# Performance work log

Hardware: AMD Instinct MI355X
Metric: run time of the kernel (lower is better)

Reference implementation:

```python
import jax, jax.numpy as jnp
import numpy as np

QUBITS = 8
EMBED_DIM = 512
FFN_DIM = 2048


def setup_inputs() -> dict:
    key = jax.random.key(0)
    k_x, k_p, k_w, k_b = jax.random.split(key, 4)
    x = jax.random.normal(k_x, (16, 4096, EMBED_DIM), dtype=jnp.float32)
    params = jax.random.normal(k_p, (QUBITS, 3), dtype=jnp.float32)
    # nn.Linear(qubits, ffn_dim): weight [ffn_dim, qubits], bias [ffn_dim]
    lim = 1.0 / np.sqrt(QUBITS)
    W = jax.random.uniform(k_w, (FFN_DIM, QUBITS), minval=-lim, maxval=lim, dtype=jnp.float32)
    b = jax.random.uniform(k_b, (FFN_DIM,), minval=-lim, maxval=lim, dtype=jnp.float32)
    return {"x": x, "params": params, "W": W, "b": b}


def reference(x, params, W, b):
    # Each qubit i: |0> -> RX(x[..., i % E]) -> RY(params[i,0]) -> RZ(params[i,1]),
    # RZ leaves <Z> unchanged.
    idx = jnp.arange(QUBITS) % x.shape[-1]          # [Q]
    z = jnp.cos(x[..., idx]) * jnp.cos(params[:, 0])  # [B,S,Q]
    return jnp.einsum('bsq,fq->bsf', z, W) + b        # [B,S,ffn_dim]
```

## Files before the change

kernel.cpp:

```cpp
#include <hip/hip_runtime.h>
#include <math.h>

#define QUBITS 8
#define EMBED 512
#define FFN 2048
#define ROWS_PER_BLOCK 32
#define THREADS 256

using f32x4 = __attribute__((ext_vector_type(4))) float;

__global__ __launch_bounds__(THREADS) void qff_kernel(
    const float* __restrict__ x, const float* __restrict__ params,
    const float* __restrict__ W, const float* __restrict__ b,
    float* __restrict__ out)
{
    __shared__ float z_lds[ROWS_PER_BLOCK][QUBITS];

    const int t = threadIdx.x;
    const long long row0 = (long long)blockIdx.x * ROWS_PER_BLOCK;

    {
        const int r = t >> 3, q = t & 7;
        const float xv = x[(row0 + r) * EMBED + q];
        const float cp = cosf(params[q * 3]);
        z_lds[r][q] = cosf(xv) * cp;
    }
    __syncthreads();

    float w[2][4][QUBITS];
    float bias[2][4];
    #pragma unroll
    for (int k = 0; k < 2; ++k) {
        const int fbase = k * 1024 + t * 4;
        #pragma unroll
        for (int j = 0; j < 4; ++j) {
            const f32x4* wp = (const f32x4*)(W + (size_t)(fbase + j) * QUBITS);
            const f32x4 w0 = wp[0], w1 = wp[1];
            w[k][j][0] = w0.x; w[k][j][1] = w0.y; w[k][j][2] = w0.z; w[k][j][3] = w0.w;
            w[k][j][4] = w1.x; w[k][j][5] = w1.y; w[k][j][6] = w1.z; w[k][j][7] = w1.w;
            bias[k][j] = b[fbase + j];
        }
    }

    float* p = out + row0 * FFN + (size_t)t * 4;

    #pragma unroll 2
    for (int r = 0; r < ROWS_PER_BLOCK; ++r) {
        float z[QUBITS];
        #pragma unroll
        for (int q = 0; q < QUBITS; ++q) z[q] = z_lds[r][q];

        #pragma unroll
        for (int k = 0; k < 2; ++k) {
            float a[4];
            #pragma unroll
            for (int j = 0; j < 4; ++j) {
                float s = bias[k][j];
                #pragma unroll
                for (int q = 0; q < QUBITS; ++q) s = fmaf(z[q], w[k][j][q], s);
                a[j] = s;
            }
            f32x4 acc;
            acc.x = a[0]; acc.y = a[1]; acc.z = a[2]; acc.w = a[3];
            *(f32x4*)(p + k * 1024) = acc;
        }
        p += FFN;
    }
}

extern "C" void kernel_launch(void* const* d_in, const int* in_sizes, int n_in,
                              void* d_out, int out_size, void* d_ws, size_t ws_size,
                              hipStream_t stream) {
    const float* x      = (const float*)d_in[0];
    const float* params = (const float*)d_in[1];
    const float* W      = (const float*)d_in[2];
    const float* b      = (const float*)d_in[3];
    float* out = (float*)d_out;

    const long long rows = (long long)in_sizes[0] / EMBED;
    const int grid = (int)(rows / ROWS_PER_BLOCK);

    qff_kernel<<<grid, THREADS, 0, stream>>>(x, params, W, b, out);
}
```

Baseline: 107.9 us.

## Split cosine prep into separate kernel and use nontemporal output stores

Adds a prep kernel that computes the 8 qubit Z expectations per row into workspace with vectorized loads. A store-focused kernel then reads these compact z values instead of doing strided x gathers and cosines. Both paths switch output writes to nontemporal stores to cut cache pollution on the 512MB output stream, and the unroll pragma is dropped. The cost is an extra launch and a small intermediate buffer round-trip; the fused path remains as a fallback when workspace is too small.

```diff
diff --git a/kernel.cpp b/kernel.cpp
--- a/kernel.cpp
+++ b/kernel.cpp
@@ -9,7 +9,81 @@
 
 using f32x4 = __attribute__((ext_vector_type(4))) float;
 
-__global__ __launch_bounds__(THREADS) void qff_kernel(
+__global__ __launch_bounds__(THREADS) void zprep_kernel(
+    const float* __restrict__ x, const float* __restrict__ params,
+    float* __restrict__ z, long long rows)
+{
+    const long long tid = (long long)blockIdx.x * THREADS + threadIdx.x;
+    const long long row = tid >> 1;
+    if (row >= rows) return;
+    const int half = (int)(tid & 1);
+
+    float cp[4];
+    #pragma unroll
+    for (int j = 0; j < 4; ++j) cp[j] = cosf(params[(half * 4 + j) * 3]);
+
+    const f32x4 xv = *(const f32x4*)(x + row * EMBED + half * 4);
+    f32x4 zv;
+    zv.x = cosf(xv.x) * cp[0];
+    zv.y = cosf(xv.y) * cp[1];
+    zv.z = cosf(xv.z) * cp[2];
+    zv.w = cosf(xv.w) * cp[3];
+    *(f32x4*)(z + row * QUBITS + half * 4) = zv;
+}
+
+__global__ __launch_bounds__(THREADS) void qff_store_kernel(
+    const float* __restrict__ z, const float* __restrict__ W,
+    const float* __restrict__ b, float* __restrict__ out)
+{
+    __shared__ float z_lds[ROWS_PER_BLOCK * QUBITS];
+
+    const int t = threadIdx.x;
+    const long long row0 = (long long)blockIdx.x * ROWS_PER_BLOCK;
+
+    z_lds[t] = z[row0 * QUBITS + t];
+    __syncthreads();
+
+    float w[2][4][QUBITS];
+    float bias[2][4];
+    #pragma unroll
+    for (int k = 0; k < 2; ++k) {
+        const int fbase = k * 1024 + t * 4;
+        #pragma unroll
+        for (int j = 0; j < 4; ++j) {
+            const f32x4* wp = (const f32x4*)(W + (size_t)(fbase + j) * QUBITS);
+            const f32x4 w0 = wp[0], w1 = wp[1];
+            w[k][j][0] = w0.x; w[k][j][1] = w0.y; w[k][j][2] = w0.z; w[k][j][3] = w0.w;
+            w[k][j][4] = w1.x; w[k][j][5] = w1.y; w[k][j][6] = w1.z; w[k][j][7] = w1.w;
+            bias[k][j] = b[fbase + j];
+        }
+    }
+
+    float* p = out + row0 * FFN + (size_t)t * 4;
+
+    for (int r = 0; r < ROWS_PER_BLOCK; ++r) {
+        float zv[QUBITS];
+        #pragma unroll
+        for (int q = 0; q < QUBITS; ++q) zv[q] = z_lds[r * QUBITS + q];
+
+        #pragma unroll
+        for (int k = 0; k < 2; ++k) {
+            float a[4];
+            #pragma unroll
+            for (int j = 0; j < 4; ++j) {
+                float s = bias[k][j];
+                #pragma unroll
+                for (int q = 0; q < QUBITS; ++q) s = fmaf(zv[q], w[k][j][q], s);
+                a[j] = s;
+            }
+            f32x4 acc;
+            acc.x = a[0]; acc.y = a[1]; acc.z = a[2]; acc.w = a[3];
+            __builtin_nontemporal_store(acc, (f32x4*)(p + k * 1024));
+        }
+        p += FFN;
+    }
+}
+
+__global__ __launch_bounds__(THREADS) void qff_fused_kernel(
     const float* __restrict__ x, const float* __restrict__ params,
     const float* __restrict__ W, const float* __restrict__ b,
     float* __restrict__ out)
@@ -18,12 +92,10 @@
 
     const int t = threadIdx.x;
     const long long row0 = (long long)blockIdx.x * ROWS_PER_BLOCK;
-
     {
         const int r = t >> 3, q = t & 7;
         const float xv = x[(row0 + r) * EMBED + q];
-        const float cp = cosf(params[q * 3]);
-        z_lds[r][q] = cosf(xv) * cp;
+        z_lds[r][q] = cosf(xv) * cosf(params[q * 3]);
     }
     __syncthreads();
 
@@ -43,13 +115,10 @@
     }
 
     float* p = out + row0 * FFN + (size_t)t * 4;
-
-    #pragma unroll 2
     for (int r = 0; r < ROWS_PER_BLOCK; ++r) {
-        float z[QUBITS];
+        float zv[QUBITS];
         #pragma unroll
-        for (int q = 0; q < QUBITS; ++q) z[q] = z_lds[r][q];
-
+        for (int q = 0; q < QUBITS; ++q) zv[q] = z_lds[r][q];
         #pragma unroll
         for (int k = 0; k < 2; ++k) {
             float a[4];
@@ -57,12 +126,12 @@
             for (int j = 0; j < 4; ++j) {
                 float s = bias[k][j];
                 #pragma unroll
-                for (int q = 0; q < QUBITS; ++q) s = fmaf(z[q], w[k][j][q], s);
+                for (int q = 0; q < QUBITS; ++q) s = fmaf(zv[q], w[k][j][q], s);
                 a[j] = s;
             }
             f32x4 acc;
             acc.x = a[0]; acc.y = a[1]; acc.z = a[2]; acc.w = a[3];
-            *(f32x4*)(p + k * 1024) = acc;
+            __builtin_nontemporal_store(acc, (f32x4*)(p + k * 1024));
         }
         p += FFN;
     }
@@ -78,7 +147,16 @@
     float* out = (float*)d_out;
 
     const long long rows = (long long)in_sizes[0] / EMBED;
-    const int grid = (int)(rows / ROWS_PER_BLOCK);
+    const size_t zbytes = (size_t)rows * QUBITS * sizeof(float);
 
-    qff_kernel<<<grid, THREADS, 0, stream>>>(x, params, W, b, out);
+    if (ws_size >= zbytes) {
+        float* z = (float*)d_ws;
+        const int grid1 = (int)((rows * 2 + THREADS - 1) / THREADS);
+        zprep_kernel<<<grid1, THREADS, 0, stream>>>(x, params, z, rows);
+        const int grid2 = (int)(rows / ROWS_PER_BLOCK);
+        qff_store_kernel<<<grid2, THREADS, 0, stream>>>(z, W, b, out);
+    } else {
+        const int grid = (int)(rows / ROWS_PER_BLOCK);
+        qff_fused_kernel<<<grid, THREADS, 0, stream>>>(x, params, W, b, out);
+    }
 }
```

Result: no change. 107.6 us (-0.3%).
